# Kernel optimization log

Hardware: AMD Instinct MI355X
Metric: run time of the kernel (lower is better)

Reference implementation:

```python
import jax, jax.numpy as jnp
import numpy as np

B, T, CNN, HW = 512, 256, 512, 7
V, H = 37, 8  # vocab_size, hidden_size


def setup_inputs() -> dict:
    key = jax.random.key(0)
    ks = jax.random.split(key, 10)
    s = 0.1
    return {
        "features": jax.random.normal(ks[0], (B, CNN, HW, HW), jnp.float32),
        "captions": jax.random.normal(ks[1], (B, T, V), jnp.float32),
        "W_in": jax.random.normal(ks[2], (V, CNN), jnp.float32) * s,
        "b_in": jax.random.normal(ks[3], (V,), jnp.float32) * s,
        "W_ih": jax.random.normal(ks[4], (4 * H, V), jnp.float32) * s,
        "W_hh": jax.random.normal(ks[5], (4 * H, H), jnp.float32) * s,
        "b_ih": jax.random.normal(ks[6], (4 * H,), jnp.float32) * s,
        "b_hh": jax.random.normal(ks[7], (4 * H,), jnp.float32) * s,
        "W_out": jax.random.normal(ks[8], (V, H), jnp.float32) * s,
        "b_out": jax.random.normal(ks[9], (V,), jnp.float32) * s,
    }


def reference(features, captions, W_in, b_in, W_ih, W_hh, b_ih, b_hh, W_out, b_out):
    # AdaptiveAvgPool2d(1) + flatten + fc_in -> [B, V]
    feat = features.mean(axis=(2, 3)) @ W_in.T + b_in
    # input at t=0 is feat, at t>0 is captions[:, t-1]; build [T, B, V] sequence
    xs = jnp.concatenate([feat[None], jnp.swapaxes(captions, 0, 1)[:-1]], axis=0)

    def step(carry, x):
        h, c = carry
        gates = x @ W_ih.T + b_ih + h @ W_hh.T + b_hh  # [B, 4H]
        i, f, g, o = jnp.split(gates, 4, axis=1)  # PyTorch LSTMCell gate order
        i = jax.nn.sigmoid(i)
        f = jax.nn.sigmoid(f)
        g = jnp.tanh(g)
        o = jax.nn.sigmoid(o)
        c = f * c + i * g
        h = o * jnp.tanh(c)
        out = jax.nn.softmax(h @ W_out.T + b_out, axis=1)  # [B, V]
        return (h, c), out

    h0 = jnp.zeros((feat.shape[0], W_hh.shape[1]), feat.dtype)
    c0 = jnp.zeros_like(h0)
    _, outs = jax.lax.scan(step, (h0, c0), xs)  # outs: [T, B, V]
    return jnp.swapaxes(outs, 0, 1)  # [B, T, V]
```

## Files before the change

kernel.cpp:

```cpp
#include <hip/hip_runtime.h>
#include <math.h>

#define BB   512
#define TT   256
#define CNNC 512
#define VV   37
#define HH   8
#define G4   32
#define CH   16
#define NCH  (TT / CH)
#define CHW  (CH * 128)

#define L2E 1.4426950408889634f

typedef float f4_t __attribute__((ext_vector_type(4)));
typedef float f2_t __attribute__((ext_vector_type(2)));

template <int CTRL>
__device__ __forceinline__ float dpp_f(float x) {
    int r = __builtin_amdgcn_update_dpp(0, __float_as_int(x), CTRL, 0xF, 0xF, true);
    return __int_as_float(r);
}

__device__ __forceinline__ float rcp_f(float x) { return __builtin_amdgcn_rcpf(x); }
__device__ __forceinline__ float exp2_f(float x) { return __builtin_amdgcn_exp2f(x); }

__device__ __forceinline__ f2_t fma2(f2_t a, f2_t b, f2_t c) {
    return __builtin_elementwise_fma(a, b, c);
}
__device__ __forceinline__ f2_t sp2(float x) { f2_t v = {x, x}; return v; }

__global__ __launch_bounds__(256) void k_feat(const float* __restrict__ features,
                                              const float* __restrict__ W_in,
                                              const float* __restrict__ b_in,
                                              float* __restrict__ featp) {
    __shared__ __align__(16) float raw[128 * 49];
    __shared__ float pooled[128];
    const int b = blockIdx.x, qt = blockIdx.y, tid = threadIdx.x;
    const f4_t* src =
        (const f4_t*)(features + (size_t)b * CNNC * 49 + qt * (128 * 49));
    f4_t* dst = (f4_t*)raw;
    for (int i = tid; i < 128 * 49 / 4; i += 256)
        dst[i] = __builtin_nontemporal_load(&src[i]);
    __syncthreads();
    if (tid < 128) {
        const float* p = raw + tid * 49;
        float s = 0.f;
        #pragma unroll
        for (int i = 0; i < 49; ++i) s += p[i];
        pooled[tid] = s;
    }
    __syncthreads();
    const int v = tid >> 2, pp = tid & 3;
    if (v < VV) {
        const float* w = W_in + v * CNNC + qt * 128 + pp * 32;
        const float* q = pooled + pp * 32;
        float s = 0.f;
        #pragma unroll
        for (int i = 0; i < 32; ++i) s += q[i] * w[i];
        s += __shfl_xor(s, 1);
        s += __shfl_xor(s, 2);
        if (pp == 0)
            featp[(qt * BB + b) * VV + v] =
                s * (1.f / 49.f) + (qt == 0 ? b_in[v] : 0.f);
    }
}

#define CAPS 1188
#define SOS  132
__global__ __launch_bounds__(256) void k_xproj(const float* __restrict__ captions,
                                               const float* __restrict__ W_ih,
                                               const float* __restrict__ b_ih,
                                               const float* __restrict__ b_hh,
                                               const float* __restrict__ featp,
                                               float* __restrict__ xproj) {
    __shared__ float W[G4 * VV];
    __shared__ float bias[G4];
    __shared__ float cap[4 * CAPS];
    __shared__ __align__(16) float so[32 * SOS];
    const int bg = blockIdx.x, tile = blockIdx.y;
    const int tid = threadIdx.x;
    for (int i = tid; i < G4 * VV; i += 256) W[i] = W_ih[i];
    if (tid < G4) bias[tid] = b_ih[tid] + b_hh[tid];

    const int t0 = tile * 32;
    const int start = (tile == 0) ? 0 : t0 - 1;
    for (int i = tid; i < 4 * 1184; i += 256) {
        const int s2 = i / 1184;
        const int off = i - s2 * 1184;
        cap[s2 * CAPS + off] = __builtin_nontemporal_load(
            &captions[((size_t)(bg * 4 + s2) * TT + start) * VV + off]);
    }
    __syncthreads();

    const int tl = tid >> 3;
    const int s  = (tid >> 1) & 3;
    const int r  = tid & 1;
    const int b  = bg * 4 + s;

    float xr[VV];
    if (tile == 0 && tl == 0) {
        #pragma unroll
        for (int v = 0; v < VV; ++v)
            xr[v] = featp[b * VV + v] + featp[(BB + b) * VV + v] +
                    featp[(2 * BB + b) * VV + v] + featp[(3 * BB + b) * VV + v];
    } else {
        const int lr = (tile == 0) ? tl - 1 : tl;
        const float* x = &cap[s * CAPS + lr * VV];
        #pragma unroll
        for (int v = 0; v < VV; ++v) xr[v] = x[v];
    }

    const int g0 = r * 16;
    float acc[16];
    #pragma unroll
    for (int g = 0; g < 16; ++g) acc[g] = bias[g0 + g];
    #pragma unroll
    for (int v = 0; v < VV; ++v) {
        const float xv = xr[v];
        #pragma unroll
        for (int g = 0; g < 16; ++g) acc[g] += xv * W[(g0 + g) * VV + v];
    }
    #pragma unroll
    for (int g = 0; g < 16; ++g) {
        const int gg = g0 + g;
        const float sc = (gg >= 16 && gg < 24) ? (-2.f * L2E) : (-L2E);
        const int word = ((gg & 15) * 4 + s) * 2 + (gg >> 4);
        so[tl * SOS + word] = acc[g] * sc;
    }
    __syncthreads();

    float* chunk = xproj + ((size_t)bg * TT + t0) * 128;
    for (int i = tid; i < 1024; i += 256) {
        const int t2 = i >> 5, rest = i & 31;
        f4_t val = *(const f4_t*)&so[t2 * SOS + rest * 4];
        *(f4_t*)&chunk[t2 * 128 + rest * 4] = val;
    }
}

#define TSTR 12
#define SSTR (CH * TSTR + 4)

#define STEP(cur, tl) do {                                                  \
    const f2_t p2 = cur[tl];                                                \
    const float ha0 = h;                                                    \
    const float ha1 = dpp_f<0x4E>(h);                                       \
    const float ha3 = dpp_f<0x141>(h);                                      \
    const float ha2 = dpp_f<0x4E>(ha3);                                     \
    const float ha7 = dpp_f<0x140>(h);                                      \
    const float ha4 = dpp_f<0x141>(ha7);                                    \
    const float ha5 = dpp_f<0x4E>(ha4);                                     \
    const float ha6 = dpp_f<0x1B>(ha7);                                     \
    f2_t acc0 = fma2(w2[0], sp2(ha0), p2);                                  \
    acc0 = fma2(w2[1], sp2(ha1), acc0);                                     \
    acc0 = fma2(w2[2], sp2(ha2), acc0);                                     \
    acc0 = fma2(w2[3], sp2(ha3), acc0);                                     \
    f2_t acc1 = w2[4] * sp2(ha4);                                           \
    acc1 = fma2(w2[5], sp2(ha5), acc1);                                     \
    acc1 = fma2(w2[6], sp2(ha6), acc1);                                     \
    acc1 = fma2(w2[7], sp2(ha7), acc1);                                     \
    const f2_t np2 = acc0 + acc1;                                           \
    const float eA = rcp_f(1.f + exp2_f(np2.x));       \
    const float uB = rcp_f(1.f + exp2_f(np2.y));   \
    const float gg = fmaf(-4.f * L2E, uB, 2.f * L2E);    \
    const float myU = r ? eA : eA * gg;           \
    const float otU = dpp_f<0xB1>(myU);                                     \
    const float fg  = r ? myU : otU;                                        \
    const float igg = r ? otU : myU;                                        \
    const float ogx = dpp_f<0xB1>(uB);                                      \
    const float og  = r ? uB : ogx;                                         \
    c = fmaf(fg, c, igg);                         \
    const float rv = rcp_f(1.f + exp2_f(c));                                \
    h = fmaf(og + og, rv, -og);                             \
    hsv[tl] = h;                                                            \
} while (0)

#define CHUNK(cur, nxt, it, pbuf) do {                                      \
    if ((it) + 1 < NCH) {                                                   \
        const f2_t* src = (const f2_t*)(xp + ((it) + 1) * CHW + roff2);     \
        _Pragma("unroll")                                                   \
        for (int tl = 0; tl < CH; ++tl) nxt[tl] = src[tl * 64];             \
        __builtin_amdgcn_sched_barrier(0);                                  \
    }                                                                       \
    _Pragma("unroll")                                                       \
    for (int tl = 0; tl < CH; ++tl) STEP(cur, tl);                          \
    if (r == 0) {                                                           \
        float* hb = &hst[((pbuf) * 4 + s4) * SSTR + j];                     \
        _Pragma("unroll")                                                   \
        for (int i = 0; i < CH; ++i) hb[i * TSTR] = hsv[i];                 \
    }                                                                       \
} while (0)

#define EMIT(pk) do {                                                       \
    const int os = lane >> 4, otl = lane & 15;                              \
    const float* hp = &hst[(((pk) & 1) * 4 + os) * SSTR + otl * TSTR];      \
    const f4_t h0 = *(const f4_t*)hp;                                       \
    const f4_t h1 = *(const f4_t*)(hp + 4);                                 \
    const f4_t* W4 = (const f4_t*)Wo;                                       \
    float z[VV];                                                            \
    float m = -1e30f;                                                       \
    _Pragma("unroll")                                                       \
    for (int v = 0; v < VV; ++v) {                                          \
        const f4_t w0 = W4[v * 2], w1 = W4[v * 2 + 1];                      \
        float sv = bo[v];                                                   \
        sv = fmaf(h0.x, w0.x, sv); sv = fmaf(h0.y, w0.y, sv);               \
        sv = fmaf(h0.z, w0.z, sv); sv = fmaf(h0.w, w0.w, sv);               \
        sv = fmaf(h1.x, w1.x, sv); sv = fmaf(h1.y, w1.y, sv);               \
        sv = fmaf(h1.z, w1.z, sv); sv = fmaf(h1.w, w1.w, sv);               \
        z[v] = sv;                                                          \
        m = fmaxf(m, sv);                                                   \
    }                                                                       \
    float sum = 0.f;                                                        \
    _Pragma("unroll")                                                       \
    for (int v = 0; v < VV; ++v) {                                          \
        z[v] = exp2_f((z[v] - m) * L2E);                                    \
        sum += z[v];                                                        \
    }                                                                       \
    const float rs = rcp_f(sum);                                            \
    const int ob = bg * 4 + os;                                             \
    const int ot = (pk) * CH + otl;                                         \
    float* op = out + ((size_t)ob * TT + ot) * VV;                          \
    _Pragma("unroll")                                                       \
    for (int v = 0; v < VV; ++v) op[v] = z[v] * rs;                         \
} while (0)

__global__ __launch_bounds__(128) void k_lstm(const float* __restrict__ W_hh,
                                              const float* __restrict__ xproj,
                                              const float* __restrict__ W_out,
                                              const float* __restrict__ b_out,
                                              float* __restrict__ out) {
    __shared__ __align__(16) float hst[2 * 4 * SSTR];
    __shared__ __align__(16) float Wo[VV * HH];
    __shared__ float bo[VV];

    const int tid  = threadIdx.x;
    const int wv   = tid >> 6;
    const int lane = tid & 63;
    const int bg   = blockIdx.x;
    const float* xp = xproj + (size_t)bg * (TT * 128);

    const int s4 = lane >> 4;
    const int q  = lane & 15;
    const int j  = q >> 1;
    const int r  = q & 1;
    const int rowA  = r * 8 + j;
    const int roff2 = (rowA * 4 + s4) * 2;

    f2_t cA[CH], cB[CH];
    float hsv[CH];
    f2_t w2[HH];

    if (wv == 0) {
        const int rowB = 16 + rowA;
        const float scA = -L2E;
        const float scB = r ? -L2E : (-2.f * L2E);
        #pragma unroll
        for (int m = 0; m < HH; ++m) {
            f2_t wp = {scA * W_hh[rowA * HH + (j ^ m)],
                       scB * W_hh[rowB * HH + (j ^ m)]};
            w2[m] = wp;
        }
        const f2_t* src = (const f2_t*)(xp + roff2);
        #pragma unroll
        for (int tl = 0; tl < CH; ++tl) cA[tl] = src[tl * 64];
    } else {
        for (int i = lane; i < VV * HH; i += 64) Wo[i] = W_out[i];
        if (lane < VV) bo[lane] = b_out[lane];
    }

    float h = 0.f, c = 0.f;

    for (int ou = 0; ou < 9; ++ou) {
        {
            const int it = ou * 2;
            if (wv == 0) {
                if (it < NCH) CHUNK(cA, cB, it, 0);
            } else if (it >= 1 && it <= NCH) {
                EMIT(it - 1);
            }
            asm volatile("s_waitcnt lgkmcnt(0)" ::: "memory");
            __builtin_amdgcn_s_barrier();
            __builtin_amdgcn_sched_barrier(0);
        }
        {
            const int it = ou * 2 + 1;
            if (it <= NCH) {
                if (wv == 0) {
                    if (it < NCH) CHUNK(cB, cA, it, 1);
                } else {
                    EMIT(it - 1);
                }
                asm volatile("s_waitcnt lgkmcnt(0)" ::: "memory");
                __builtin_amdgcn_s_barrier();
                __builtin_amdgcn_sched_barrier(0);
            }
        }
    }
}

extern "C" void kernel_launch(void* const* d_in, const int* in_sizes, int n_in,
                              void* d_out, int out_size, void* d_ws, size_t ws_size,
                              hipStream_t stream) {
    const float* features = (const float*)d_in[0];
    const float* captions = (const float*)d_in[1];
    const float* W_in     = (const float*)d_in[2];
    const float* b_in     = (const float*)d_in[3];
    const float* W_ih     = (const float*)d_in[4];
    const float* W_hh     = (const float*)d_in[5];
    const float* b_ih     = (const float*)d_in[6];
    const float* b_hh     = (const float*)d_in[7];
    const float* W_out    = (const float*)d_in[8];
    const float* b_out    = (const float*)d_in[9];
    float* out = (float*)d_out;

    float* ws    = (float*)d_ws;
    float* featp = ws;
    float* xproj = ws + 81920;

    k_feat <<<dim3(BB, 4),  256, 0, stream>>>(features, W_in, b_in, featp);
    k_xproj<<<dim3(128, 8), 256, 0, stream>>>(captions, W_ih, b_ih, b_hh, featp, xproj);
    k_lstm <<<128,          128, 0, stream>>>(W_hh, xproj, W_out, b_out, out);
}
```

Measured before the change: 192.6 us.

## Stage softmax outputs in LDS for coalesced stores; use Newton reciprocals

```diff
diff --git a/kernel.cpp b/kernel.cpp
--- a/kernel.cpp
+++ b/kernel.cpp
@@ -24,6 +24,20 @@
 
 __device__ __forceinline__ float rcp_f(float x) { return __builtin_amdgcn_rcpf(x); }
 __device__ __forceinline__ float exp2_f(float x) { return __builtin_amdgcn_exp2f(x); }
+
+__device__ __forceinline__ float nrcp2(float x) {
+    float y = __int_as_float(0x7EF127EA - __float_as_int(x));
+    y = y * fmaf(-x, y, 2.f);
+    y = y * fmaf(-x, y, 2.f);
+    return y;
+}
+__device__ __forceinline__ float nrcp3(float x) {
+    float y = __int_as_float(0x7EF127EA - __float_as_int(x));
+    y = y * fmaf(-x, y, 2.f);
+    y = y * fmaf(-x, y, 2.f);
+    y = y * fmaf(-x, y, 2.f);
+    return y;
+}
 
 __device__ __forceinline__ f2_t fma2(f2_t a, f2_t b, f2_t c) {
     return __builtin_elementwise_fma(a, b, c);
@@ -160,8 +174,10 @@
     acc1 = fma2(w2[6], sp2(ha6), acc1);                                     \
     acc1 = fma2(w2[7], sp2(ha7), acc1);                                     \
     const f2_t np2 = acc0 + acc1;                                           \
-    const float eA = rcp_f(1.f + exp2_f(np2.x));       \
-    const float uB = rcp_f(1.f + exp2_f(np2.y));   \
+    const float xA = 1.f + exp2_f(np2.x);                                   \
+    const float xB = 1.f + exp2_f(np2.y);                                   \
+    const float eA = nrcp2(xA);                        \
+    const float uB = nrcp2(xB);                    \
     const float gg = fmaf(-4.f * L2E, uB, 2.f * L2E);    \
     const float myU = r ? eA : eA * gg;           \
     const float otU = dpp_f<0xB1>(myU);                                     \
@@ -170,7 +186,8 @@
     const float ogx = dpp_f<0xB1>(uB);                                      \
     const float og  = r ? uB : ogx;                                         \
     c = fmaf(fg, c, igg);                         \
-    const float rv = rcp_f(1.f + exp2_f(c));                                \
+    const float xC = 1.f + exp2_f(c);                                       \
+    const float rv = nrcp3(xC);                                             \
     h = fmaf(og + og, rv, -og);                             \
     hsv[tl] = h;                                                            \
 } while (0)
@@ -217,11 +234,16 @@
         sum += z[v];                                                        \
     }                                                                       \
     const float rs = rcp_f(sum);                                            \
-    const int ob = bg * 4 + os;                                             \
-    const int ot = (pk) * CH + otl;                                         \
-    float* op = out + ((size_t)ob * TT + ot) * VV;                          \
-    _Pragma("unroll")                                                       \
-    for (int v = 0; v < VV; ++v) op[v] = z[v] * rs;                         \
+    _Pragma("unroll")                                                       \
+    for (int v = 0; v < VV; ++v) zst[lane * VV + v] = z[v] * rs;            \
+                   \
+    _Pragma("unroll")                                                       \
+    for (int sq = 0; sq < 4; ++sq) {                                        \
+        const f4_t* sp = (const f4_t*)&zst[sq * (CH * VV)];                 \
+        f4_t* gp = (f4_t*)(out + ((size_t)(bg * 4 + sq) * TT + (pk) * CH) * VV); \
+        for (int k2 = lane; k2 < CH * VV / 4; k2 += 64)                     \
+            __builtin_nontemporal_store(sp[k2], &gp[k2]);                   \
+    }                                                                       \
 } while (0)
 
 __global__ __launch_bounds__(128) void k_lstm(const float* __restrict__ W_hh,
@@ -230,6 +252,7 @@
                                               const float* __restrict__ b_out,
                                               float* __restrict__ out) {
     __shared__ __align__(16) float hst[2 * 4 * SSTR];
+    __shared__ __align__(16) float zst[64 * VV];
     __shared__ __align__(16) float Wo[VV * HH];
     __shared__ float bo[VV];
 
```

Result: slower. 198.2 us (+2.9%).

## Interleave two independent batch groups per recurrence wave to hide latency

Applied to the files above, without the earlier changes.

```diff
diff --git a/kernel.cpp b/kernel.cpp
--- a/kernel.cpp
+++ b/kernel.cpp
@@ -9,7 +9,7 @@
 #define G4   32
 #define CH   16
 #define NCH  (TT / CH)
-#define CHW  (CH * 128)
+#define CHW  (CH * 256)
 
 #define L2E 1.4426950408889634f
 
@@ -130,18 +130,19 @@
     }
     __syncthreads();
 
-    float* chunk = xproj + ((size_t)bg * TT + t0) * 128;
+    float* chunk =
+        xproj + ((size_t)(bg >> 1) * TT + t0) * 256 + (bg & 1) * 128;
     for (int i = tid; i < 1024; i += 256) {
         const int t2 = i >> 5, rest = i & 31;
         f4_t val = *(const f4_t*)&so[t2 * SOS + rest * 4];
-        *(f4_t*)&chunk[t2 * 128 + rest * 4] = val;
+        *(f4_t*)&chunk[t2 * 256 + rest * 4] = val;
     }
 }
 
 #define TSTR 12
 #define SSTR (CH * TSTR + 4)
 
-#define STEP(cur, tl) do {                                                  \
+#define STEPX(cur, tl, h, c, hsv) do {                                      \
     const f2_t p2 = cur[tl];                                                \
     const float ha0 = h;                                                    \
     const float ha1 = dpp_f<0x4E>(h);                                       \
@@ -175,25 +176,36 @@
     hsv[tl] = h;                                                            \
 } while (0)
 
-#define CHUNK(cur, nxt, it, pbuf) do {                                      \
+#define CHUNK2(curP, curQ, nxtP, nxtQ, it, pbuf) do {                       \
     if ((it) + 1 < NCH) {                                                   \
-        const f2_t* src = (const f2_t*)(xp + ((it) + 1) * CHW + roff2);     \
+        const f2_t* sp = (const f2_t*)xp + (size_t)((it) + 1) * (CHW / 2) + roff1; \
         _Pragma("unroll")                                                   \
-        for (int tl = 0; tl < CH; ++tl) nxt[tl] = src[tl * 64];             \
+        for (int tl = 0; tl < CH; ++tl) {                                   \
+            nxtP[tl] = sp[tl * 128];                                        \
+            nxtQ[tl] = sp[tl * 128 + 64];                                   \
+        }                                                                   \
         __builtin_amdgcn_sched_barrier(0);                                  \
     }                                                                       \
     _Pragma("unroll")                                                       \
-    for (int tl = 0; tl < CH; ++tl) STEP(cur, tl);                          \
+    for (int tl = 0; tl < CH; ++tl) {                                       \
+        STEPX(curP, tl, hP, cP, hsvP);                                      \
+        STEPX(curQ, tl, hQ, cQ, hsvQ);                                      \
+    }                                                                       \
     if (r == 0) {                                                           \
-        float* hb = &hst[((pbuf) * 4 + s4) * SSTR + j];                     \
+        float* hbP = &hst[((pbuf) * 8 + s4) * SSTR + j];                    \
+        float* hbQ = &hst[((pbuf) * 8 + 4 + s4) * SSTR + j];                \
         _Pragma("unroll")                                                   \
-        for (int i = 0; i < CH; ++i) hb[i * TSTR] = hsv[i];                 \
+        for (int i = 0; i < CH; ++i) {                                      \
+            hbP[i * TSTR] = hsvP[i];                                        \
+            hbQ[i * TSTR] = hsvQ[i];                                        \
+        }                                                                   \
     }                                                                       \
 } while (0)
 
 #define EMIT(pk) do {                                                       \
-    const int os = lane >> 4, otl = lane & 15;                              \
-    const float* hp = &hst[(((pk) & 1) * 4 + os) * SSTR + otl * TSTR];      \
+    const int row = (wv - 1) * 64 + lane;                       \
+    const int os = row >> 4, otl = row & 15;                                \
+    const float* hp = &hst[(((pk) & 1) * 8 + os) * SSTR + otl * TSTR];      \
     const f4_t h0 = *(const f4_t*)hp;                                       \
     const f4_t h1 = *(const f4_t*)(hp + 4);                                 \
     const f4_t* W4 = (const f4_t*)Wo;                                       \
@@ -217,19 +229,19 @@
         sum += z[v];                                                        \
     }                                                                       \
     const float rs = rcp_f(sum);                                            \
-    const int ob = bg * 4 + os;                                             \
+    const int ob = bg * 8 + os;                                             \
     const int ot = (pk) * CH + otl;                                         \
     float* op = out + ((size_t)ob * TT + ot) * VV;                          \
     _Pragma("unroll")                                                       \
     for (int v = 0; v < VV; ++v) op[v] = z[v] * rs;                         \
 } while (0)
 
-__global__ __launch_bounds__(128) void k_lstm(const float* __restrict__ W_hh,
+__global__ __launch_bounds__(192) void k_lstm(const float* __restrict__ W_hh,
                                               const float* __restrict__ xproj,
                                               const float* __restrict__ W_out,
                                               const float* __restrict__ b_out,
                                               float* __restrict__ out) {
-    __shared__ __align__(16) float hst[2 * 4 * SSTR];
+    __shared__ __align__(16) float hst[2 * 8 * SSTR];
     __shared__ __align__(16) float Wo[VV * HH];
     __shared__ float bo[VV];
 
@@ -237,17 +249,17 @@
     const int wv   = tid >> 6;
     const int lane = tid & 63;
     const int bg   = blockIdx.x;
-    const float* xp = xproj + (size_t)bg * (TT * 128);
+    const float* xp = xproj + (size_t)bg * (TT * 256);
 
     const int s4 = lane >> 4;
     const int q  = lane & 15;
     const int j  = q >> 1;
     const int r  = q & 1;
     const int rowA  = r * 8 + j;
-    const int roff2 = (rowA * 4 + s4) * 2;
-
-    f2_t cA[CH], cB[CH];
-    float hsv[CH];
+    const int roff1 = rowA * 4 + s4;
+
+    f2_t cPA[CH], cPB[CH], cQA[CH], cQB[CH];
+    float hsvP[CH], hsvQ[CH];
     f2_t w2[HH];
 
     if (wv == 0) {
@@ -260,21 +272,25 @@
                        scB * W_hh[rowB * HH + (j ^ m)]};
             w2[m] = wp;
         }
-        const f2_t* src = (const f2_t*)(xp + roff2);
-        #pragma unroll
-        for (int tl = 0; tl < CH; ++tl) cA[tl] = src[tl * 64];
+        const f2_t* sp = (const f2_t*)xp + roff1;
+        #pragma unroll
+        for (int tl = 0; tl < CH; ++tl) {
+            cPA[tl] = sp[tl * 128];
+            cQA[tl] = sp[tl * 128 + 64];
+        }
     } else {
-        for (int i = lane; i < VV * HH; i += 64) Wo[i] = W_out[i];
-        if (lane < VV) bo[lane] = b_out[lane];
-    }
-
-    float h = 0.f, c = 0.f;
+        const int l2 = tid - 64;
+        for (int i = l2; i < VV * HH; i += 128) Wo[i] = W_out[i];
+        if (l2 < VV) bo[l2] = b_out[l2];
+    }
+
+    float hP = 0.f, cP = 0.f, hQ = 0.f, cQ = 0.f;
 
     for (int ou = 0; ou < 9; ++ou) {
         {
             const int it = ou * 2;
             if (wv == 0) {
-                if (it < NCH) CHUNK(cA, cB, it, 0);
+                if (it < NCH) CHUNK2(cPA, cQA, cPB, cQB, it, 0);
             } else if (it >= 1 && it <= NCH) {
                 EMIT(it - 1);
             }
@@ -286,7 +302,7 @@
             const int it = ou * 2 + 1;
             if (it <= NCH) {
                 if (wv == 0) {
-                    if (it < NCH) CHUNK(cB, cA, it, 1);
+                    if (it < NCH) CHUNK2(cPB, cQB, cPA, cQA, it, 1);
                 } else {
                     EMIT(it - 1);
                 }
@@ -319,5 +335,5 @@
 
     k_feat <<<dim3(BB, 4),  256, 0, stream>>>(features, W_in, b_in, featp);
     k_xproj<<<dim3(128, 8), 256, 0, stream>>>(captions, W_ih, b_ih, b_hh, featp, xproj);
-    k_lstm <<<128,          128, 0, stream>>>(W_hh, xproj, W_out, b_out, out);
-}
+    k_lstm <<<64,           192, 0, stream>>>(W_hh, xproj, W_out, b_out, out);
+}
```

Result: slower. 206.3 us (+7.1%).

## Fuse input projection into LSTM kernel with producer waves and LDS ring

Applied to the files above, without the earlier changes.

```diff
diff --git a/kernel.cpp b/kernel.cpp
--- a/kernel.cpp
+++ b/kernel.cpp
@@ -9,7 +9,6 @@
 #define G4   32
 #define CH   16
 #define NCH  (TT / CH)
-#define CHW  (CH * 128)
 
 #define L2E 1.4426950408889634f
 
@@ -66,83 +65,18 @@
     }
 }
 
-#define CAPS 1188
-#define SOS  132
-__global__ __launch_bounds__(256) void k_xproj(const float* __restrict__ captions,
-                                               const float* __restrict__ W_ih,
-                                               const float* __restrict__ b_ih,
-                                               const float* __restrict__ b_hh,
-                                               const float* __restrict__ featp,
-                                               float* __restrict__ xproj) {
-    __shared__ float W[G4 * VV];
-    __shared__ float bias[G4];
-    __shared__ float cap[4 * CAPS];
-    __shared__ __align__(16) float so[32 * SOS];
-    const int bg = blockIdx.x, tile = blockIdx.y;
-    const int tid = threadIdx.x;
-    for (int i = tid; i < G4 * VV; i += 256) W[i] = W_ih[i];
-    if (tid < G4) bias[tid] = b_ih[tid] + b_hh[tid];
-
-    const int t0 = tile * 32;
-    const int start = (tile == 0) ? 0 : t0 - 1;
-    for (int i = tid; i < 4 * 1184; i += 256) {
-        const int s2 = i / 1184;
-        const int off = i - s2 * 1184;
-        cap[s2 * CAPS + off] = __builtin_nontemporal_load(
-            &captions[((size_t)(bg * 4 + s2) * TT + start) * VV + off]);
-    }
-    __syncthreads();
-
-    const int tl = tid >> 3;
-    const int s  = (tid >> 1) & 3;
-    const int r  = tid & 1;
-    const int b  = bg * 4 + s;
-
-    float xr[VV];
-    if (tile == 0 && tl == 0) {
-        #pragma unroll
-        for (int v = 0; v < VV; ++v)
-            xr[v] = featp[b * VV + v] + featp[(BB + b) * VV + v] +
-                    featp[(2 * BB + b) * VV + v] + featp[(3 * BB + b) * VV + v];
-    } else {
-        const int lr = (tile == 0) ? tl - 1 : tl;
-        const float* x = &cap[s * CAPS + lr * VV];
-        #pragma unroll
-        for (int v = 0; v < VV; ++v) xr[v] = x[v];
-    }
-
-    const int g0 = r * 16;
-    float acc[16];
-    #pragma unroll
-    for (int g = 0; g < 16; ++g) acc[g] = bias[g0 + g];
-    #pragma unroll
-    for (int v = 0; v < VV; ++v) {
-        const float xv = xr[v];
-        #pragma unroll
-        for (int g = 0; g < 16; ++g) acc[g] += xv * W[(g0 + g) * VV + v];
-    }
-    #pragma unroll
-    for (int g = 0; g < 16; ++g) {
-        const int gg = g0 + g;
-        const float sc = (gg >= 16 && gg < 24) ? (-2.f * L2E) : (-L2E);
-        const int word = ((gg & 15) * 4 + s) * 2 + (gg >> 4);
-        so[tl * SOS + word] = acc[g] * sc;
-    }
-    __syncthreads();
-
-    float* chunk = xproj + ((size_t)bg * TT + t0) * 128;
-    for (int i = tid; i < 1024; i += 256) {
-        const int t2 = i >> 5, rest = i & 31;
-        f4_t val = *(const f4_t*)&so[t2 * SOS + rest * 4];
-        *(f4_t*)&chunk[t2 * 128 + rest * 4] = val;
-    }
-}
-
 #define TSTR 12
 #define SSTR (CH * TSTR + 4)
-
-#define STEP(cur, tl) do {                                                  \
-    const f2_t p2 = cur[tl];                                                \
+#define RSTR 132
+#define RING_T (CH * RSTR)
+
+#define BAR() do {                                                          \
+    asm volatile("s_waitcnt lgkmcnt(0)" ::: "memory");                      \
+    __builtin_amdgcn_s_barrier();                                           \
+    __builtin_amdgcn_sched_barrier(0);                                      \
+} while (0)
+
+#define STEP(p2) do {                                                       \
     const float ha0 = h;                                                    \
     const float ha1 = dpp_f<0x4E>(h);                                       \
     const float ha3 = dpp_f<0x141>(h);                                      \
@@ -172,23 +106,49 @@
     c = fmaf(fg, c, igg);                         \
     const float rv = rcp_f(1.f + exp2_f(c));                                \
     h = fmaf(og + og, rv, -og);                             \
-    hsv[tl] = h;                                                            \
-} while (0)
-
-#define CHUNK(cur, nxt, it, pbuf) do {                                      \
-    if ((it) + 1 < NCH) {                                                   \
-        const f2_t* src = (const f2_t*)(xp + ((it) + 1) * CHW + roff2);     \
-        _Pragma("unroll")                                                   \
-        for (int tl = 0; tl < CH; ++tl) nxt[tl] = src[tl * 64];             \
-        __builtin_amdgcn_sched_barrier(0);                                  \
-    }                                                                       \
-    _Pragma("unroll")                                                       \
-    for (int tl = 0; tl < CH; ++tl) STEP(cur, tl);                          \
+} while (0)
+
+#define SCHUNK(it) do {                                                     \
+    const float* base = &ring[((it) % 3) * RING_T] + roff2w;                \
+    float hsv[CH];                                                          \
+    _Pragma("unroll")                                                       \
+    for (int tl = 0; tl < CH; ++tl) {                                       \
+        const f2_t p2 = *(const f2_t*)&base[tl * RSTR];                     \
+        STEP(p2);                                                           \
+        hsv[tl] = h;                                                        \
+    }                                                                       \
     if (r == 0) {                                                           \
-        float* hb = &hst[((pbuf) * 4 + s4) * SSTR + j];                     \
+        float* hb = &hst[(((it) & 1) * 4 + s4) * SSTR + j];                 \
         _Pragma("unroll")                                                   \
         for (int i = 0; i < CH; ++i) hb[i * TSTR] = hsv[i];                 \
     }                                                                       \
+} while (0)
+
+#define PRODUCE_BODY(pk)                                                    \
+    float acc[16];                                                          \
+    _Pragma("unroll")                                                       \
+    for (int g = 0; g < 16; ++g) acc[g] = bs[g];                            \
+    _Pragma("unroll")                                                       \
+    for (int v = 0; v < VV; ++v) {                                          \
+        const float xv = xr[v];                                             \
+        _Pragma("unroll")                                                   \
+        for (int g = 0; g < 16; ++g) acc[g] += xv * Wih[(g0 + g) * VV + v]; \
+    }                                                                       \
+    float* dst = &ring[((pk) % 3) * RING_T + ptl * RSTR];                   \
+    _Pragma("unroll")                                                       \
+    for (int g = 0; g < 16; ++g) {                                          \
+        const int gg = g0 + g;                                              \
+        const float sc = (gg >= 16 && gg < 24) ? (-2.f * L2E) : (-L2E);     \
+        dst[((gg & 15) * 4 + ps) * 2 + (gg >> 4)] = acc[g] * sc;            \
+    }
+
+#define PRODUCE(pk) do {                    \
+    const int t = (pk) * CH + ptl;                                          \
+    const float* x = captions + ((size_t)pb * TT + (t - 1)) * VV;           \
+    float xr[VV];                                                           \
+    _Pragma("unroll")                                                       \
+    for (int v = 0; v < VV; ++v) xr[v] = x[v];                              \
+    PRODUCE_BODY(pk)                                                        \
 } while (0)
 
 #define EMIT(pk) do {                                                       \
@@ -224,12 +184,18 @@
     for (int v = 0; v < VV; ++v) op[v] = z[v] * rs;                         \
 } while (0)
 
-__global__ __launch_bounds__(128) void k_lstm(const float* __restrict__ W_hh,
-                                              const float* __restrict__ xproj,
+__global__ __launch_bounds__(256) void k_lstm(const float* __restrict__ W_hh,
+                                              const float* __restrict__ captions,
+                                              const float* __restrict__ W_ih,
+                                              const float* __restrict__ b_ih,
+                                              const float* __restrict__ b_hh,
+                                              const float* __restrict__ featp,
                                               const float* __restrict__ W_out,
                                               const float* __restrict__ b_out,
                                               float* __restrict__ out) {
+    __shared__ __align__(16) float ring[3 * RING_T];
     __shared__ __align__(16) float hst[2 * 4 * SSTR];
+    __shared__ __align__(16) float Wih[G4 * VV];
     __shared__ __align__(16) float Wo[VV * HH];
     __shared__ float bo[VV];
 
@@ -237,18 +203,23 @@
     const int wv   = tid >> 6;
     const int lane = tid & 63;
     const int bg   = blockIdx.x;
-    const float* xp = xproj + (size_t)bg * (TT * 128);
 
     const int s4 = lane >> 4;
     const int q  = lane & 15;
     const int j  = q >> 1;
     const int r  = q & 1;
-    const int rowA  = r * 8 + j;
-    const int roff2 = (rowA * 4 + s4) * 2;
-
-    f2_t cA[CH], cB[CH];
-    float hsv[CH];
+    const int rowA   = r * 8 + j;
+    const int roff2w = (rowA * 4 + s4) * 2;
+
+    const int p   = tid & 127;
+    const int ptl = p >> 3;
+    const int ps  = (p >> 1) & 3;
+    const int pr  = p & 1;
+    const int g0  = pr * 16;
+    const int pb  = bg * 4 + ps;
+
     f2_t w2[HH];
+    float bs[16];
 
     if (wv == 0) {
         const int rowB = 16 + rowA;
@@ -260,41 +231,44 @@
                        scB * W_hh[rowB * HH + (j ^ m)]};
             w2[m] = wp;
         }
-        const f2_t* src = (const f2_t*)(xp + roff2);
-        #pragma unroll
-        for (int tl = 0; tl < CH; ++tl) cA[tl] = src[tl * 64];
-    } else {
+    } else if (wv == 1) {
         for (int i = lane; i < VV * HH; i += 64) Wo[i] = W_out[i];
         if (lane < VV) bo[lane] = b_out[lane];
-    }
+    } else {
+        for (int i = p; i < G4 * VV; i += 128) Wih[i] = W_ih[i];
+        #pragma unroll
+        for (int g = 0; g < 16; ++g) bs[g] = b_ih[g0 + g] + b_hh[g0 + g];
+    }
+    BAR();
+
+    if (wv >= 2) {
+        float xr[VV];
+        if (ptl == 0) {
+            #pragma unroll
+            for (int v = 0; v < VV; ++v)
+                xr[v] = featp[pb * VV + v] + featp[(BB + pb) * VV + v] +
+                        featp[(2 * BB + pb) * VV + v] +
+                        featp[(3 * BB + pb) * VV + v];
+        } else {
+            const float* x = captions + ((size_t)pb * TT + (ptl - 1)) * VV;
+            #pragma unroll
+            for (int v = 0; v < VV; ++v) xr[v] = x[v];
+        }
+        PRODUCE_BODY(0)
+    }
+    BAR();
 
     float h = 0.f, c = 0.f;
 
-    for (int ou = 0; ou < 9; ++ou) {
-        {
-            const int it = ou * 2;
-            if (wv == 0) {
-                if (it < NCH) CHUNK(cA, cB, it, 0);
-            } else if (it >= 1 && it <= NCH) {
-                EMIT(it - 1);
-            }
-            asm volatile("s_waitcnt lgkmcnt(0)" ::: "memory");
-            __builtin_amdgcn_s_barrier();
-            __builtin_amdgcn_sched_barrier(0);
+    for (int it = 0; it < NCH + 1; ++it) {
+        if (wv == 0) {
+            if (it < NCH) SCHUNK(it);
+        } else if (wv == 1) {
+            if (it >= 1) EMIT(it - 1);
+        } else {
+            if (it < NCH - 1) PRODUCE(it + 1);
         }
-        {
-            const int it = ou * 2 + 1;
-            if (it <= NCH) {
-                if (wv == 0) {
-                    if (it < NCH) CHUNK(cB, cA, it, 1);
-                } else {
-                    EMIT(it - 1);
-                }
-                asm volatile("s_waitcnt lgkmcnt(0)" ::: "memory");
-                __builtin_amdgcn_s_barrier();
-                __builtin_amdgcn_sched_barrier(0);
-            }
-        }
+        BAR();
     }
 }
 
@@ -313,11 +287,9 @@
     const float* b_out    = (const float*)d_in[9];
     float* out = (float*)d_out;
 
-    float* ws    = (float*)d_ws;
-    float* featp = ws;
-    float* xproj = ws + 81920;
-
-    k_feat <<<dim3(BB, 4),  256, 0, stream>>>(features, W_in, b_in, featp);
-    k_xproj<<<dim3(128, 8), 256, 0, stream>>>(captions, W_ih, b_ih, b_hh, featp, xproj);
-    k_lstm <<<128,          128, 0, stream>>>(W_hh, xproj, W_out, b_out, out);
-}
+    float* featp = (float*)d_ws;
+
+    k_feat<<<dim3(BB, 4), 256, 0, stream>>>(features, W_in, b_in, featp);
+    k_lstm<<<128,         256, 0, stream>>>(W_hh, captions, W_ih, b_ih, b_hh,
+                                            featp, W_out, b_out, out);
+}
```

New measurement: 174.5 us. -9.4%, faster.
